# Kernel optimization log

Hardware: AMD Instinct MI355X
Metric: run time of the kernel (lower is better)

## Reference

```python
import jax, jax.numpy as jnp
import numpy as np
import math

D = 2048
NH = 16
HD = D // NH
MULT = 4
EPS = 1e-6


def rmsnorm(x, g):
    norm = jax.lax.rsqrt(jnp.mean(x * x, axis=-1, keepdims=True) + EPS)
    return g * x * norm


def setup_inputs() -> dict:
    key = jax.random.key(0)
    ks = jax.random.split(key, 8)
    s = 0.02  # keep activations in a sane range
    return {
        "x": jax.random.normal(ks[0], (2, 2048, D), dtype=jnp.float32),
        "g1": jnp.ones((D,), dtype=jnp.float32),
        "wq": jax.random.normal(ks[1], (D, D), dtype=jnp.float32) * s,
        "wk": jax.random.normal(ks[2], (D, D), dtype=jnp.float32) * s,
        "wv": jax.random.normal(ks[3], (D, D), dtype=jnp.float32) * s,
        "wo": jax.random.normal(ks[4], (D, D), dtype=jnp.float32) * s,
        "g2": jnp.ones((D,), dtype=jnp.float32),
        "w_up": jax.random.normal(ks[5], (2 * D * MULT, D), dtype=jnp.float32) * s,
        "w_down": jax.random.normal(ks[6], (D, D * MULT), dtype=jnp.float32) * s,
    }


def reference(x, g1, wq, wk, wv, wo, g2, w_up, w_down):
    B, T, _ = x.shape
    # --- causal self-attention with pre-RMSNorm ---
    h = rmsnorm(x, g1)
    q = (h @ wq.T).reshape(B, T, NH, HD).transpose(0, 2, 1, 3)  # [B,H,T,hd]
    k = (h @ wk.T).reshape(B, T, NH, HD).transpose(0, 2, 1, 3)
    v = (h @ wv.T).reshape(B, T, NH, HD).transpose(0, 2, 1, 3)
    att = jnp.einsum("bhtd,bhsd->bhts", q, k) / math.sqrt(HD)  # [B,H,T,T]
    neg = jnp.finfo(att.dtype).min
    causal = jnp.triu(jnp.full((T, T), neg, dtype=att.dtype), k=1)
    att = att + causal
    w = jax.nn.softmax(att, axis=-1)
    z = jnp.einsum("bhts,bhsd->bhtd", w, v)  # [B,H,T,hd]
    z = z.transpose(0, 2, 1, 3).reshape(B, T, D)
    x = x + z @ wo.T
    # --- SwiGLU-style FFN (GELU gate) with pre-RMSNorm ---
    h2 = rmsnorm(x, g2)
    uv = h2 @ w_up.T  # [B,T,2*D*MULT]
    u, vgate = jnp.split(uv, 2, axis=-1)
    ff = (jax.nn.gelu(u, approximate=False) * vgate) @ w_down.T
    return x + ff
```

## Files before the change

### kernel.cpp

```cpp
#include <hip/hip_runtime.h>
#include <math.h>

typedef __bf16 bf16_t;
typedef __bf16 bf16x8 __attribute__((ext_vector_type(8)));
typedef __bf16 bf16x4 __attribute__((ext_vector_type(4)));
typedef float f32x4 __attribute__((ext_vector_type(4)));

#define D_MODEL 2048
#define N_HEADS 16
#define HEAD_D 128
#define SEQ 2048
#define NTOK 4096
#define DFF 8192
#define UPN 16384

#define GLDS16(g, l) __builtin_amdgcn_global_load_lds( \
    (const __attribute__((address_space(1))) void*)(g), \
    (__attribute__((address_space(3))) void*)(l), 16, 0, 0)

#define MFMA16(a, b, c) __builtin_amdgcn_mfma_f32_16x16x32_bf16((a), (b), (c), 0, 0, 0)

__global__ __launch_bounds__(256) void cvt_bf16_kernel(const float* __restrict__ in,
                                                       bf16_t* __restrict__ out, long n4) {
    long i = (long)blockIdx.x * 256 + threadIdx.x;
    long stride = (long)gridDim.x * 256;
    for (; i < n4; i += stride) {
        float4 f = ((const float4*)in)[i];
        bf16x4 v;
        v[0] = (bf16_t)f.x; v[1] = (bf16_t)f.y; v[2] = (bf16_t)f.z; v[3] = (bf16_t)f.w;
        ((bf16x4*)out)[i] = v;
    }
}

__global__ __launch_bounds__(256) void rmsnorm_kernel(const float* __restrict__ x,
                                                      const float* __restrict__ g,
                                                      bf16_t* __restrict__ out) {
    int row = blockIdx.x;
    const float* xr = x + (size_t)row * D_MODEL;
    int c0 = threadIdx.x * 8;
    float4 a = *(const float4*)&xr[c0];
    float4 b = *(const float4*)&xr[c0 + 4];
    float ss = a.x*a.x + a.y*a.y + a.z*a.z + a.w*a.w
             + b.x*b.x + b.y*b.y + b.z*b.z + b.w*b.w;
    #pragma unroll
    for (int off = 1; off < 64; off <<= 1) ss += __shfl_xor(ss, off);
    __shared__ float red[4];
    if ((threadIdx.x & 63) == 0) red[threadIdx.x >> 6] = ss;
    __syncthreads();
    float norm = rsqrtf((red[0] + red[1] + red[2] + red[3]) * (1.f / D_MODEL) + 1e-6f);
    float4 ga = *(const float4*)&g[c0];
    float4 gb = *(const float4*)&g[c0 + 4];
    bf16x8 o;
    o[0] = (bf16_t)(a.x * ga.x * norm); o[1] = (bf16_t)(a.y * ga.y * norm);
    o[2] = (bf16_t)(a.z * ga.z * norm); o[3] = (bf16_t)(a.w * ga.w * norm);
    o[4] = (bf16_t)(b.x * gb.x * norm); o[5] = (bf16_t)(b.y * gb.y * norm);
    o[6] = (bf16_t)(b.z * gb.z * norm); o[7] = (bf16_t)(b.w * gb.w * norm);
    *(bf16x8*)&out[(size_t)row * D_MODEL + c0] = o;
}

__global__ __launch_bounds__(256) void combine3_kernel(const float* __restrict__ r,
        const float* __restrict__ p0, const float* __restrict__ p1,
        float* __restrict__ out, long n4) {
    long i = (long)blockIdx.x * 256 + threadIdx.x;
    long stride = (long)gridDim.x * 256;
    for (; i < n4; i += stride) {
        float4 a = ((const float4*)r)[i];
        float4 b = ((const float4*)p0)[i];
        float4 c = ((const float4*)p1)[i];
        float4 o; o.x = a.x+b.x+c.x; o.y = a.y+b.y+c.y; o.z = a.z+b.z+c.z; o.w = a.w+b.w+c.w;
        ((float4*)out)[i] = o;
    }
}

template<int MODE, int KSPLIT>
__global__ __launch_bounds__(512, 2)
void gemm256(const bf16_t* __restrict__ A, const bf16_t* __restrict__ W,
             void* __restrict__ o0, void* __restrict__ o1, void* __restrict__ o2,
             const float* __restrict__ res, int nbx, int K)
{
    __shared__ __align__(16) bf16_t ldsA[2 * 2 * 8192];
    __shared__ __align__(16) bf16_t ldsB[2 * 2 * 8192];
    const int tid = threadIdx.x;
    const int wave = tid >> 6, lane = tid & 63;
    const int lr = lane & 15, lg = lane >> 4;
    const int wm = wave >> 2, wn = wave & 3;

    const int nwg = gridDim.x, bid = blockIdx.x;
    const int cpx = nwg >> 3;
    const int s = (bid & 7) * cpx + (bid >> 3);
    const int by = s & 15, bx = s >> 4;
    const int bm0 = by * 256;
    const int bn0 = (MODE == 2) ? bx * 128 : bx * 256;
    const int z = (KSPLIT == 2) ? blockIdx.z : 0;
    const int Keff = K / KSPLIT, koff = z * Keff;

    const int rl = wave * 16 + (lane >> 2);
    const int gsw = ((lane & 3) ^ ((rl >> 1) & 3)) * 8;
    const bf16_t* asrc = A + (size_t)(bm0 + rl) * K + koff + gsw;
    const bf16_t* bsrc;
    size_t bstep2;
    if constexpr (MODE == 2) {
        int grp = rl >> 6, wi = rl & 63;
        int brow = (wi < 32) ? (bn0 + grp * 32 + wi) : (DFF + bn0 + grp * 32 + (wi - 32));
        bsrc = W + (size_t)brow * K + koff + gsw;
        bstep2 = (size_t)64 * K;
    } else {
        bsrc = W + (size_t)(bn0 + rl) * K + koff + gsw;
        bstep2 = (size_t)128 * K;
    }

    auto stA = [&](int t, int kh) {
        char* d = (char*)ldsA + (((t & 1) * 2 + kh) * 16384) + wave * 1024 + lane * 16;
        const bf16_t* sp = asrc + (size_t)t * 64 + kh * 32;
        GLDS16(sp, d);
        GLDS16(sp + (size_t)128 * K, d + 8192);
    };
    auto stB = [&](int t, int kh) {
        char* d = (char*)ldsB + (((t & 1) * 2 + kh) * 16384) + wave * 1024 + lane * 16;
        const bf16_t* sp = bsrc + (size_t)t * 64 + kh * 32;
        GLDS16(sp, d);
        GLDS16(sp + bstep2, d + 8192);
    };

    f32x4 acc[8][4] = {};
    const int xg = (lg ^ ((lr >> 1) & 3)) * 8;
    const int NKT = Keff >> 6;

    stA(0, 0); stB(0, 0); stA(0, 1); stB(0, 1); stA(1, 0); stB(1, 0);
    asm volatile("s_waitcnt vmcnt(8)" ::: "memory");
    __builtin_amdgcn_s_barrier();

#define TILE_BODY(T, S1, S2, W1, W2)                                                    \
    {                                                                                   \
        const int t_ = (T);                                                             \
        const bf16_t* Ab = ldsA + ((t_ & 1) * 2) * 8192;                                \
        const bf16_t* Bb = ldsB + ((t_ & 1) * 2) * 8192;                                \
        bf16x8 a0[4], a1[4], b0[4], b1[4];                                              \
                                                                      \
        _Pragma("unroll")                                                               \
        for (int i = 0; i < 4; ++i)                                                     \
            a0[i] = *(const bf16x8*)&Ab[(wm * 128 + i * 16 + lr) * 32 + xg];            \
        _Pragma("unroll")                                                               \
        for (int n = 0; n < 4; ++n)                                                     \
            b0[n] = *(const bf16x8*)&Bb[(wn * 64 + n * 16 + lr) * 32 + xg];             \
        if (S1) stA(t_ + 1, 1);                                                         \
        __builtin_amdgcn_s_setprio(1);                                                  \
        _Pragma("unroll")                                                               \
        for (int i = 0; i < 4; ++i)                                                     \
            _Pragma("unroll")                                                           \
            for (int n = 0; n < 4; ++n)                                                 \
                acc[i][n] = MFMA16(a0[i], b0[n], acc[i][n]);                            \
        __builtin_amdgcn_s_setprio(0);                                                  \
                                                                      \
        _Pragma("unroll")                                                               \
        for (int i = 0; i < 4; ++i)                                                     \
            a1[i] = *(const bf16x8*)&Ab[(wm * 128 + (i + 4) * 16 + lr) * 32 + xg];      \
        if (S1) stB(t_ + 1, 1);                                                         \
        __builtin_amdgcn_s_setprio(1);                                                  \
        _Pragma("unroll")                                                               \
        for (int i = 0; i < 4; ++i)                                                     \
            _Pragma("unroll")                                                           \
            for (int n = 0; n < 4; ++n)                                                 \
                acc[i + 4][n] = MFMA16(a1[i], b0[n], acc[i + 4][n]);                    \
        __builtin_amdgcn_s_setprio(0);                                                  \
        asm volatile("s_waitcnt vmcnt(" W1 ")" ::: "memory");                           \
        __builtin_amdgcn_s_barrier();                                                   \
                                                                      \
        _Pragma("unroll")                                                               \
        for (int i = 0; i < 4; ++i)                                                     \
            a0[i] = *(const bf16x8*)&Ab[8192 + (wm * 128 + i * 16 + lr) * 32 + xg];     \
        _Pragma("unroll")                                                               \
        for (int n = 0; n < 4; ++n)                                                     \
            b1[n] = *(const bf16x8*)&Bb[8192 + (wn * 64 + n * 16 + lr) * 32 + xg];      \
        if (S2) stA(t_ + 2, 0);                                                         \
        __builtin_amdgcn_s_setprio(1);                                                  \
        _Pragma("unroll")                                                               \
        for (int i = 0; i < 4; ++i)                                                     \
            _Pragma("unroll")                                                           \
            for (int n = 0; n < 4; ++n)                                                 \
                acc[i][n] = MFMA16(a0[i], b1[n], acc[i][n]);                            \
        __builtin_amdgcn_s_setprio(0);                                                  \
                                                                      \
        _Pragma("unroll")                                                               \
        for (int i = 0; i < 4; ++i)                                                     \
            a1[i] = *(const bf16x8*)&Ab[8192 + (wm * 128 + (i + 4) * 16 + lr) * 32 + xg]; \
        if (S2) stB(t_ + 2, 0);                                                         \
        __builtin_amdgcn_s_setprio(1);                                                  \
        _Pragma("unroll")                                                               \
        for (int i = 0; i < 4; ++i)                                                     \
            _Pragma("unroll")                                                           \
            for (int n = 0; n < 4; ++n)                                                 \
                acc[i + 4][n] = MFMA16(a1[i], b1[n], acc[i + 4][n]);                    \
        __builtin_amdgcn_s_setprio(0);                                                  \
        asm volatile("s_waitcnt vmcnt(" W2 ")" ::: "memory");                           \
        __builtin_amdgcn_s_barrier();                                                   \
    }

    for (int t = 0; t < NKT - 2; ++t) TILE_BODY(t, true, true, "8", "8");
    TILE_BODY(NKT - 2, true, false, "8", "4");
    TILE_BODY(NKT - 1, false, false, "0", "0");
#undef TILE_BODY

    if constexpr (MODE == 0) {
        const float qs = 0.08838834764831845f;
        const int th = bn0 >> 11;
        #pragma unroll
        for (int m = 0; m < 8; ++m) {
            int grow = bm0 + wm * 128 + m * 16 + lg * 4;
            #pragma unroll
            for (int n = 0; n < 4; ++n) {
                int gcol = bn0 + wn * 64 + n * 16 + lr;
                int c = gcol & 2047;
                if (th == 0) {
                    #pragma unroll
                    for (int r = 0; r < 4; ++r)
                        ((bf16_t*)o0)[(size_t)(grow + r) * D_MODEL + c] = (bf16_t)(acc[m][n][r] * qs);
                } else if (th == 1) {
                    #pragma unroll
                    for (int r = 0; r < 4; ++r)
                        ((bf16_t*)o1)[(size_t)(grow + r) * D_MODEL + c] = (bf16_t)acc[m][n][r];
                } else {
                    int hh = c >> 7, d = c & 127;
                    int bb = grow >> 11, t0 = grow & 2047;
                    bf16x4 st;
                    #pragma unroll
                    for (int r = 0; r < 4; ++r) st[r] = (bf16_t)acc[m][n][r];
                    *(bf16x4*)&((bf16_t*)o2)[((size_t)(bb * N_HEADS + hh) * HEAD_D + d) * SEQ + t0] = st;
                }
            }
        }
    } else if constexpr (MODE == 1) {
        float* po = (KSPLIT == 2) ? ((float*)o0 + (size_t)z * NTOK * D_MODEL) : (float*)o0;
        #pragma unroll
        for (int m = 0; m < 8; ++m) {
            int grow = bm0 + wm * 128 + m * 16 + lg * 4;
            #pragma unroll
            for (int n = 0; n < 4; ++n) {
                int gcol = bn0 + wn * 64 + n * 16 + lr;
                #pragma unroll
                for (int r = 0; r < 4; ++r) {
                    size_t idx = (size_t)(grow + r) * D_MODEL + gcol;
                    if (KSPLIT == 2) po[idx] = acc[m][n][r];
                    else             po[idx] = res[idx] + acc[m][n][r];
                }
            }
        }
    } else {
        #pragma unroll
        for (int m = 0; m < 8; ++m) {
            int grow = bm0 + wm * 128 + m * 16 + lg * 4;
            #pragma unroll
            for (int n = 0; n < 2; ++n) {
                int gcol = bn0 + wn * 32 + n * 16 + lr;
                #pragma unroll
                for (int r = 0; r < 4; ++r) {
                    float u = acc[m][n][r], vg = acc[m][n + 2][r];
                    float ge = 0.5f * u * (1.f + erff(u * 0.70710678118654752f));
                    ((bf16_t*)o0)[(size_t)(grow + r) * DFF + gcol] = (bf16_t)(ge * vg);
                }
            }
        }
    }
}

__global__ __launch_bounds__(256)
void attn_kernel(const bf16_t* __restrict__ Q, const bf16_t* __restrict__ K,
                 const bf16_t* __restrict__ Vt, bf16_t* __restrict__ Z)
{
    const int qt = gridDim.x - 1 - blockIdx.x;
    const int h = blockIdx.y, b = blockIdx.z;
    const int q0 = qt * 64;
    const int tid = threadIdx.x, wave = tid >> 6, lane = tid & 63;
    const int lr = lane & 15, lg = lane >> 4;

    __shared__ __align__(16) bf16_t Qs[64 * 136];
    __shared__ __align__(16) bf16_t Ks[64 * 136];
    __shared__ __align__(16) bf16_t Vts[128 * 72];
    __shared__ __align__(16) bf16_t Ps[4][16 * 72];

    const size_t base = ((size_t)b * SEQ) * D_MODEL + (size_t)h * HEAD_D;
    const size_t vbase = (size_t)(b * N_HEADS + h) * HEAD_D * SEQ;

    const int kr = tid >> 4, kc = (tid & 15) * 8;
    const int vdr = tid >> 3, vc = (tid & 7) * 8;

    #pragma unroll
    for (int i = 0; i < 4; ++i)
        *(uint4*)&Qs[(kr + i * 16) * 136 + kc] =
            *(const uint4*)&Q[base + (size_t)(q0 + kr + i * 16) * D_MODEL + kc];

    uint4 k0g, k1g, k2g, k3g, v0g, v1g, v2g, v3g;
    const bf16_t* Kb = K + base + (size_t)kr * D_MODEL + kc;
    const bf16_t* Vb = Vt + vbase + (size_t)vdr * SEQ + vc;
    auto loadKV = [&](int kt) {
        const bf16_t* kp = Kb + (size_t)kt * 64 * D_MODEL;
        k0g = *(const uint4*)kp;
        k1g = *(const uint4*)(kp + (size_t)16 * D_MODEL);
        k2g = *(const uint4*)(kp + (size_t)32 * D_MODEL);
        k3g = *(const uint4*)(kp + (size_t)48 * D_MODEL);
        const bf16_t* vp = Vb + kt * 64;
        v0g = *(const uint4*)vp;
        v1g = *(const uint4*)(vp + (size_t)32 * SEQ);
        v2g = *(const uint4*)(vp + (size_t)64 * SEQ);
        v3g = *(const uint4*)(vp + (size_t)96 * SEQ);
    };
    loadKV(0);

    f32x4 o[8] = {};
    float mrun[4], lrun[4];
    #pragma unroll
    for (int r = 0; r < 4; ++r) { mrun[r] = -1e30f; lrun[r] = 0.f; }

    for (int kt = 0; kt <= qt; ++kt) {
        __syncthreads();
        *(uint4*)&Ks[kr * 136 + kc] = k0g;
        *(uint4*)&Ks[(kr + 16) * 136 + kc] = k1g;
        *(uint4*)&Ks[(kr + 32) * 136 + kc] = k2g;
        *(uint4*)&Ks[(kr + 48) * 136 + kc] = k3g;
        *(uint4*)&Vts[vdr * 72 + vc] = v0g;
        *(uint4*)&Vts[(vdr + 32) * 72 + vc] = v1g;
        *(uint4*)&Vts[(vdr + 64) * 72 + vc] = v2g;
        *(uint4*)&Vts[(vdr + 96) * 72 + vc] = v3g;
        __syncthreads();
        if (kt < qt) loadKV(kt + 1);

        f32x4 sv[4] = {};
        #pragma unroll
        for (int kk = 0; kk < 4; ++kk) {
            bf16x8 aq = *(const bf16x8*)&Qs[(wave * 16 + lr) * 136 + kk * 32 + lg * 8];
            #pragma unroll
            for (int nb = 0; nb < 4; ++nb) {
                bf16x8 bk = *(const bf16x8*)&Ks[(nb * 16 + lr) * 136 + kk * 32 + lg * 8];
                sv[nb] = MFMA16(aq, bk, sv[nb]);
            }
        }
        if (kt == qt) {
            #pragma unroll
            for (int nb = 0; nb < 4; ++nb)
                #pragma unroll
                for (int r = 0; r < 4; ++r) {
                    int qrel = 16 * wave + lg * 4 + r;
                    int krel = nb * 16 + lr;
                    if (krel > qrel) sv[nb][r] = -1e30f;
                }
        }
        float resc[4];
        bool defer_all = true;
        #pragma unroll
        for (int r = 0; r < 4; ++r) {
            float mx = fmaxf(fmaxf(sv[0][r], sv[1][r]), fmaxf(sv[2][r], sv[3][r]));
            #pragma unroll
            for (int off = 1; off < 16; off <<= 1) mx = fmaxf(mx, __shfl_xor(mx, off));
            bool defer = __all(mx - mrun[r] <= 8.f);
            float mnew = defer ? mrun[r] : fmaxf(mrun[r], mx);
            resc[r] = defer ? 1.f : __expf(mrun[r] - mnew);
            defer_all &= defer;
            float sum = 0.f;
            #pragma unroll
            for (int nb = 0; nb < 4; ++nb) {
                float p = __expf(sv[nb][r] - mnew);
                sv[nb][r] = p;
                sum += p;
            }
            #pragma unroll
            for (int off = 1; off < 16; off <<= 1) sum += __shfl_xor(sum, off);
            lrun[r] = lrun[r] * resc[r] + sum;
            mrun[r] = mnew;
        }
        if (!defer_all) {
            #pragma unroll
            for (int ob = 0; ob < 8; ++ob)
                #pragma unroll
                for (int r = 0; r < 4; ++r) o[ob][r] *= resc[r];
        }
        #pragma unroll
        for (int nb = 0; nb < 4; ++nb)
            #pragma unroll
            for (int r = 0; r < 4; ++r)
                Ps[wave][(lg * 4 + r) * 72 + nb * 16 + lr] = (bf16_t)sv[nb][r];
        #pragma unroll
        for (int kk = 0; kk < 2; ++kk) {
            bf16x8 ap = *(const bf16x8*)&Ps[wave][lr * 72 + kk * 32 + lg * 8];
            #pragma unroll
            for (int ob = 0; ob < 8; ++ob) {
                bf16x8 bv = *(const bf16x8*)&Vts[(ob * 16 + lr) * 72 + kk * 32 + lg * 8];
                o[ob] = MFMA16(ap, bv, o[ob]);
            }
        }
    }
    #pragma unroll
    for (int r = 0; r < 4; ++r) lrun[r] = 1.f / lrun[r];
    #pragma unroll
    for (int ob = 0; ob < 8; ++ob)
        #pragma unroll
        for (int r = 0; r < 4; ++r) {
            int t = q0 + 16 * wave + lg * 4 + r;
            Z[base + (size_t)t * D_MODEL + ob * 16 + lr] = (bf16_t)(o[ob][r] * lrun[r]);
        }
}

extern "C" void kernel_launch(void* const* d_in, const int* in_sizes, int n_in,
                              void* d_out, int out_size, void* d_ws, size_t ws_size,
                              hipStream_t stream)
{
    const float* x   = (const float*)d_in[0];
    const float* g1  = (const float*)d_in[1];
    const float* wq  = (const float*)d_in[2];
    const float* wk  = (const float*)d_in[3];
    const float* wv  = (const float*)d_in[4];
    const float* wo  = (const float*)d_in[5];
    const float* g2  = (const float*)d_in[6];
    const float* wup = (const float*)d_in[7];
    const float* wdn = (const float*)d_in[8];
    float* out = (float*)d_out;

    char* wsp = (char*)d_ws;
    size_t off = 0;
    auto alloc = [&](size_t bytes) { void* p = wsp + off; off += (bytes + 255) & ~255ull; return p; };
    bf16_t* wq_b  = (bf16_t*)alloc((size_t)D_MODEL * D_MODEL * 2);
    bf16_t* wk_b  = (bf16_t*)alloc((size_t)D_MODEL * D_MODEL * 2);
    bf16_t* wv_b  = (bf16_t*)alloc((size_t)D_MODEL * D_MODEL * 2);
    bf16_t* wo_b  = (bf16_t*)alloc((size_t)D_MODEL * D_MODEL * 2);
    bf16_t* wup_b = (bf16_t*)alloc((size_t)UPN * D_MODEL * 2);
    bf16_t* wdn_b = (bf16_t*)alloc((size_t)D_MODEL * DFF * 2);
    bf16_t* h_b   = (bf16_t*)alloc((size_t)NTOK * D_MODEL * 2);
    bf16_t* q_b   = (bf16_t*)alloc((size_t)NTOK * D_MODEL * 2);
    bf16_t* k_b   = (bf16_t*)alloc((size_t)NTOK * D_MODEL * 2);
    bf16_t* vt_b  = (bf16_t*)alloc((size_t)NTOK * D_MODEL * 2);
    bf16_t* z_b   = (bf16_t*)alloc((size_t)NTOK * D_MODEL * 2);
    float*  x1    = (float*) alloc((size_t)NTOK * D_MODEL * 4);
    bf16_t* h2_b  = (bf16_t*)alloc((size_t)NTOK * D_MODEL * 2);
    bf16_t* act_b = (bf16_t*)alloc((size_t)NTOK * DFF * 2);
    float* pbuf = (float*)h_b;

    auto cvt = [&](const float* in, bf16_t* outb, long n) {
        long n4 = n / 4;
        long nb = (n4 + 255) / 256;
        int blocks = nb > 2048 ? 2048 : (int)nb;
        cvt_bf16_kernel<<<blocks, 256, 0, stream>>>(in, outb, n4);
    };
    cvt(wq,  wq_b,  (long)D_MODEL * D_MODEL);
    cvt(wk,  wk_b,  (long)D_MODEL * D_MODEL);
    cvt(wv,  wv_b,  (long)D_MODEL * D_MODEL);
    cvt(wo,  wo_b,  (long)D_MODEL * D_MODEL);
    cvt(wup, wup_b, (long)UPN * D_MODEL);
    cvt(wdn, wdn_b, (long)D_MODEL * DFF);

    rmsnorm_kernel<<<NTOK, 256, 0, stream>>>(x, g1, h_b);

    gemm256<0, 1><<<24 * 16, 512, 0, stream>>>(h_b, wq_b, q_b, k_b, vt_b, nullptr, 24, D_MODEL);

    attn_kernel<<<dim3(SEQ / 64, N_HEADS, 2), 256, 0, stream>>>(q_b, k_b, vt_b, z_b);

    gemm256<1, 2><<<dim3(8 * 16, 1, 2), 512, 0, stream>>>(z_b, wo_b, pbuf, nullptr, nullptr, nullptr, 8, D_MODEL);
    combine3_kernel<<<2048, 256, 0, stream>>>(x, pbuf, pbuf + (size_t)NTOK * D_MODEL, x1,
                                              (long)NTOK * D_MODEL / 4);

    rmsnorm_kernel<<<NTOK, 256, 0, stream>>>(x1, g2, h2_b);

    gemm256<2, 1><<<64 * 16, 512, 0, stream>>>(h2_b, wup_b, act_b, nullptr, nullptr, nullptr, 64, D_MODEL);

    gemm256<1, 2><<<dim3(8 * 16, 1, 2), 512, 0, stream>>>(act_b, wdn_b, pbuf, nullptr, nullptr, nullptr, 8, DFF);
    combine3_kernel<<<2048, 256, 0, stream>>>(x1, pbuf, pbuf + (size_t)NTOK * D_MODEL, out,
                                              (long)NTOK * D_MODEL / 4);
}
```

Measured before the change: 963.4 us.

## Store split-K partials in bf16, fuse residual add with RMSNorm, widen attention query tile

Split-K GEMM partial outputs are now written as bf16 rather than fp32, which halves the traffic for the partial buffers and their readback in the combine kernels. The first residual combine is fused with the second RMSNorm into one row kernel, removing one launch and one full pass over x1. The attention kernel now handles 128 query rows per block as two 64-row halves that share each K/V tile load, and the V tile's LDS row pitch changes from 72 to 68. Rounding the partials to bf16 before summing costs accuracy in the residual stream, and the larger attention tile raises register and LDS use.

```diff
diff --git a/kernel.cpp b/kernel.cpp
--- a/kernel.cpp
+++ b/kernel.cpp
@@ -59,17 +59,67 @@
 }
 
 __global__ __launch_bounds__(256) void combine3_kernel(const float* __restrict__ r,
-        const float* __restrict__ p0, const float* __restrict__ p1,
-        float* __restrict__ out, long n4) {
+        const bf16_t* __restrict__ p0, const bf16_t* __restrict__ p1,
+        float* __restrict__ out, long n8) {
     long i = (long)blockIdx.x * 256 + threadIdx.x;
     long stride = (long)gridDim.x * 256;
-    for (; i < n4; i += stride) {
-        float4 a = ((const float4*)r)[i];
-        float4 b = ((const float4*)p0)[i];
-        float4 c = ((const float4*)p1)[i];
-        float4 o; o.x = a.x+b.x+c.x; o.y = a.y+b.y+c.y; o.z = a.z+b.z+c.z; o.w = a.w+b.w+c.w;
-        ((float4*)out)[i] = o;
-    }
+    for (; i < n8; i += stride) {
+        size_t e = (size_t)i * 8;
+        float4 a0 = *(const float4*)&r[e];
+        float4 a1 = *(const float4*)&r[e + 4];
+        bf16x8 b0 = *(const bf16x8*)&p0[e];
+        bf16x8 b1 = *(const bf16x8*)&p1[e];
+        float4 o0, o1;
+        o0.x = a0.x + (float)b0[0] + (float)b1[0];
+        o0.y = a0.y + (float)b0[1] + (float)b1[1];
+        o0.z = a0.z + (float)b0[2] + (float)b1[2];
+        o0.w = a0.w + (float)b0[3] + (float)b1[3];
+        o1.x = a1.x + (float)b0[4] + (float)b1[4];
+        o1.y = a1.y + (float)b0[5] + (float)b1[5];
+        o1.z = a1.z + (float)b0[6] + (float)b1[6];
+        o1.w = a1.w + (float)b0[7] + (float)b1[7];
+        *(float4*)&out[e] = o0;
+        *(float4*)&out[e + 4] = o1;
+    }
+}
+
+__global__ __launch_bounds__(256) void combine_rms_kernel(const float* __restrict__ r,
+        const bf16_t* __restrict__ p0, const bf16_t* __restrict__ p1,
+        const float* __restrict__ g, float* __restrict__ x1, bf16_t* __restrict__ h2) {
+    int row = blockIdx.x;
+    size_t rb = (size_t)row * D_MODEL;
+    int c0 = threadIdx.x * 8;
+    float4 a0 = *(const float4*)&r[rb + c0];
+    float4 a1 = *(const float4*)&r[rb + c0 + 4];
+    bf16x8 b0 = *(const bf16x8*)&p0[rb + c0];
+    bf16x8 b1 = *(const bf16x8*)&p1[rb + c0];
+    float v0 = a0.x + (float)b0[0] + (float)b1[0];
+    float v1 = a0.y + (float)b0[1] + (float)b1[1];
+    float v2 = a0.z + (float)b0[2] + (float)b1[2];
+    float v3 = a0.w + (float)b0[3] + (float)b1[3];
+    float v4 = a1.x + (float)b0[4] + (float)b1[4];
+    float v5 = a1.y + (float)b0[5] + (float)b1[5];
+    float v6 = a1.z + (float)b0[6] + (float)b1[6];
+    float v7 = a1.w + (float)b0[7] + (float)b1[7];
+    float4 w0; w0.x = v0; w0.y = v1; w0.z = v2; w0.w = v3;
+    float4 w1; w1.x = v4; w1.y = v5; w1.z = v6; w1.w = v7;
+    *(float4*)&x1[rb + c0] = w0;
+    *(float4*)&x1[rb + c0 + 4] = w1;
+    float ss = v0*v0 + v1*v1 + v2*v2 + v3*v3 + v4*v4 + v5*v5 + v6*v6 + v7*v7;
+    #pragma unroll
+    for (int off = 1; off < 64; off <<= 1) ss += __shfl_xor(ss, off);
+    __shared__ float red[4];
+    if ((threadIdx.x & 63) == 0) red[threadIdx.x >> 6] = ss;
+    __syncthreads();
+    float norm = rsqrtf((red[0] + red[1] + red[2] + red[3]) * (1.f / D_MODEL) + 1e-6f);
+    float4 ga = *(const float4*)&g[c0];
+    float4 gb = *(const float4*)&g[c0 + 4];
+    bf16x8 o;
+    o[0] = (bf16_t)(v0 * ga.x * norm); o[1] = (bf16_t)(v1 * ga.y * norm);
+    o[2] = (bf16_t)(v2 * ga.z * norm); o[3] = (bf16_t)(v3 * ga.w * norm);
+    o[4] = (bf16_t)(v4 * gb.x * norm); o[5] = (bf16_t)(v5 * gb.y * norm);
+    o[6] = (bf16_t)(v6 * gb.z * norm); o[7] = (bf16_t)(v7 * gb.w * norm);
+    *(bf16x8*)&h2[rb + c0] = o;
 }
 
 template<int MODE, int KSPLIT>
@@ -230,7 +280,7 @@
             }
         }
     } else if constexpr (MODE == 1) {
-        float* po = (KSPLIT == 2) ? ((float*)o0 + (size_t)z * NTOK * D_MODEL) : (float*)o0;
+        bf16_t* po = (bf16_t*)o0 + (size_t)z * NTOK * D_MODEL;
         #pragma unroll
         for (int m = 0; m < 8; ++m) {
             int grow = bm0 + wm * 128 + m * 16 + lg * 4;
@@ -240,8 +290,7 @@
                 #pragma unroll
                 for (int r = 0; r < 4; ++r) {
                     size_t idx = (size_t)(grow + r) * D_MODEL + gcol;
-                    if (KSPLIT == 2) po[idx] = acc[m][n][r];
-                    else             po[idx] = res[idx] + acc[m][n][r];
+                    po[idx] = (bf16_t)acc[m][n][r];
                 }
             }
         }
@@ -263,19 +312,64 @@
     }
 }
 
+#define SM_PV(svv, mr, lrr, oo)                                                         \
+    {                                                                                   \
+        float resc_[4]; bool dall_ = true;                                              \
+        _Pragma("unroll")                                                               \
+        for (int r = 0; r < 4; ++r) {                                                   \
+            float mx = fmaxf(fmaxf(svv[0][r], svv[1][r]), fmaxf(svv[2][r], svv[3][r]));  \
+            _Pragma("unroll")                                                           \
+            for (int off = 1; off < 16; off <<= 1) mx = fmaxf(mx, __shfl_xor(mx, off)); \
+            bool defer = __all(mx - mr[r] <= 8.f);                                      \
+            float mnew = defer ? mr[r] : fmaxf(mr[r], mx);                              \
+            resc_[r] = defer ? 1.f : __expf(mr[r] - mnew);                              \
+            dall_ &= defer;                                                             \
+            float sum = 0.f;                                                            \
+            _Pragma("unroll")                                                           \
+            for (int nb = 0; nb < 4; ++nb) {                                            \
+                float p = __expf(svv[nb][r] - mnew);                                    \
+                svv[nb][r] = p; sum += p;                                               \
+            }                                                                           \
+            _Pragma("unroll")                                                           \
+            for (int off = 1; off < 16; off <<= 1) sum += __shfl_xor(sum, off);         \
+            lrr[r] = lrr[r] * resc_[r] + sum; mr[r] = mnew;                             \
+        }                                                                               \
+        if (!dall_) {                                                                   \
+            _Pragma("unroll")                                                           \
+            for (int ob = 0; ob < 8; ++ob)                                              \
+                _Pragma("unroll")                                                       \
+                for (int r = 0; r < 4; ++r) oo[ob][r] *= resc_[r];                      \
+        }                                                                               \
+        _Pragma("unroll")                                                               \
+        for (int nb = 0; nb < 4; ++nb)                                                  \
+            _Pragma("unroll")                                                           \
+            for (int r = 0; r < 4; ++r)                                                 \
+                Ps[wave][(lg * 4 + r) * 72 + nb * 16 + lr] = (bf16_t)svv[nb][r];        \
+        _Pragma("unroll")                                                               \
+        for (int kk = 0; kk < 2; ++kk) {                                                \
+            bf16x8 ap = *(const bf16x8*)&Ps[wave][lr * 72 + kk * 32 + lg * 8];          \
+            _Pragma("unroll")                                                           \
+            for (int ob = 0; ob < 8; ++ob) {                                            \
+                bf16x8 bv = *(const bf16x8*)&Vts[(ob * 16 + lr) * 68 + kk * 32 + lg * 8]; \
+                oo[ob] = MFMA16(ap, bv, oo[ob]);                                        \
+            }                                                                           \
+        }                                                                               \
+    }
+
 __global__ __launch_bounds__(256)
 void attn_kernel(const bf16_t* __restrict__ Q, const bf16_t* __restrict__ K,
                  const bf16_t* __restrict__ Vt, bf16_t* __restrict__ Z)
 {
-    const int qt = gridDim.x - 1 - blockIdx.x;
+    const int qb = gridDim.x - 1 - blockIdx.x;
     const int h = blockIdx.y, b = blockIdx.z;
-    const int q0 = qt * 64;
+    const int q0 = qb * 128;
+    const int ktmax = 2 * qb + 1;
     const int tid = threadIdx.x, wave = tid >> 6, lane = tid & 63;
     const int lr = lane & 15, lg = lane >> 4;
 
-    __shared__ __align__(16) bf16_t Qs[64 * 136];
+    __shared__ __align__(16) bf16_t Qs[128 * 136];
     __shared__ __align__(16) bf16_t Ks[64 * 136];
-    __shared__ __align__(16) bf16_t Vts[128 * 72];
+    __shared__ __align__(16) bf16_t Vts[128 * 68];
     __shared__ __align__(16) bf16_t Ps[4][16 * 72];
 
     const size_t base = ((size_t)b * SEQ) * D_MODEL + (size_t)h * HEAD_D;
@@ -285,7 +379,7 @@
     const int vdr = tid >> 3, vc = (tid & 7) * 8;
 
     #pragma unroll
-    for (int i = 0; i < 4; ++i)
+    for (int i = 0; i < 8; ++i)
         *(uint4*)&Qs[(kr + i * 16) * 136 + kc] =
             *(const uint4*)&Q[base + (size_t)(q0 + kr + i * 16) * D_MODEL + kc];
 
@@ -306,98 +400,83 @@
     };
     loadKV(0);
 
-    f32x4 o[8] = {};
-    float mrun[4], lrun[4];
+    f32x4 oL[8] = {}, oH[8] = {};
+    float mL[4], lL[4], mH[4], lH[4];
     #pragma unroll
-    for (int r = 0; r < 4; ++r) { mrun[r] = -1e30f; lrun[r] = 0.f; }
-
-    for (int kt = 0; kt <= qt; ++kt) {
+    for (int r = 0; r < 4; ++r) { mL[r] = -1e30f; lL[r] = 0.f; mH[r] = -1e30f; lH[r] = 0.f; }
+
+    for (int kt = 0; kt <= ktmax; ++kt) {
         __syncthreads();
         *(uint4*)&Ks[kr * 136 + kc] = k0g;
         *(uint4*)&Ks[(kr + 16) * 136 + kc] = k1g;
         *(uint4*)&Ks[(kr + 32) * 136 + kc] = k2g;
         *(uint4*)&Ks[(kr + 48) * 136 + kc] = k3g;
-        *(uint4*)&Vts[vdr * 72 + vc] = v0g;
-        *(uint4*)&Vts[(vdr + 32) * 72 + vc] = v1g;
-        *(uint4*)&Vts[(vdr + 64) * 72 + vc] = v2g;
-        *(uint4*)&Vts[(vdr + 96) * 72 + vc] = v3g;
+        *(uint4*)&Vts[vdr * 68 + vc] = v0g;
+        *(uint4*)&Vts[(vdr + 32) * 68 + vc] = v1g;
+        *(uint4*)&Vts[(vdr + 64) * 68 + vc] = v2g;
+        *(uint4*)&Vts[(vdr + 96) * 68 + vc] = v3g;
         __syncthreads();
-        if (kt < qt) loadKV(kt + 1);
-
-        f32x4 sv[4] = {};
-        #pragma unroll
-        for (int kk = 0; kk < 4; ++kk) {
-            bf16x8 aq = *(const bf16x8*)&Qs[(wave * 16 + lr) * 136 + kk * 32 + lg * 8];
+        if (kt < ktmax) loadKV(kt + 1);
+
+        if (kt < ktmax) {
+            f32x4 sv[4] = {};
             #pragma unroll
-            for (int nb = 0; nb < 4; ++nb) {
-                bf16x8 bk = *(const bf16x8*)&Ks[(nb * 16 + lr) * 136 + kk * 32 + lg * 8];
-                sv[nb] = MFMA16(aq, bk, sv[nb]);
-            }
+            for (int kk = 0; kk < 4; ++kk) {
+                bf16x8 aq = *(const bf16x8*)&Qs[(wave * 16 + lr) * 136 + kk * 32 + lg * 8];
+                #pragma unroll
+                for (int nb = 0; nb < 4; ++nb) {
+                    bf16x8 bk = *(const bf16x8*)&Ks[(nb * 16 + lr) * 136 + kk * 32 + lg * 8];
+                    sv[nb] = MFMA16(aq, bk, sv[nb]);
+                }
+            }
+            if (kt == ktmax - 1) {
+                #pragma unroll
+                for (int nb = 0; nb < 4; ++nb)
+                    #pragma unroll
+                    for (int r = 0; r < 4; ++r) {
+                        int qrel = 16 * wave + lg * 4 + r;
+                        int krel = nb * 16 + lr;
+                        if (krel > qrel) sv[nb][r] = -1e30f;
+                    }
+            }
+            SM_PV(sv, mL, lL, oL)
         }
-        if (kt == qt) {
+        {
+            f32x4 sv[4] = {};
             #pragma unroll
-            for (int nb = 0; nb < 4; ++nb)
+            for (int kk = 0; kk < 4; ++kk) {
+                bf16x8 aq = *(const bf16x8*)&Qs[(64 + wave * 16 + lr) * 136 + kk * 32 + lg * 8];
                 #pragma unroll
-                for (int r = 0; r < 4; ++r) {
-                    int qrel = 16 * wave + lg * 4 + r;
-                    int krel = nb * 16 + lr;
-                    if (krel > qrel) sv[nb][r] = -1e30f;
+                for (int nb = 0; nb < 4; ++nb) {
+                    bf16x8 bk = *(const bf16x8*)&Ks[(nb * 16 + lr) * 136 + kk * 32 + lg * 8];
+                    sv[nb] = MFMA16(aq, bk, sv[nb]);
                 }
+            }
+            if (kt == ktmax) {
+                #pragma unroll
+                for (int nb = 0; nb < 4; ++nb)
+                    #pragma unroll
+                    for (int r = 0; r < 4; ++r) {
+                        int qrel = 16 * wave + lg * 4 + r;
+                        int krel = nb * 16 + lr;
+                        if (krel > qrel) sv[nb][r] = -1e30f;
+                    }
+            }
+            SM_PV(sv, mH, lH, oH)
         }
-        float resc[4];
-        bool defer_all = true;
-        #pragma unroll
-        for (int r = 0; r < 4; ++r) {
-            float mx = fmaxf(fmaxf(sv[0][r], sv[1][r]), fmaxf(sv[2][r], sv[3][r]));
-            #pragma unroll
-            for (int off = 1; off < 16; off <<= 1) mx = fmaxf(mx, __shfl_xor(mx, off));
-            bool defer = __all(mx - mrun[r] <= 8.f);
-            float mnew = defer ? mrun[r] : fmaxf(mrun[r], mx);
-            resc[r] = defer ? 1.f : __expf(mrun[r] - mnew);
-            defer_all &= defer;
-            float sum = 0.f;
-            #pragma unroll
-            for (int nb = 0; nb < 4; ++nb) {
-                float p = __expf(sv[nb][r] - mnew);
-                sv[nb][r] = p;
-                sum += p;
-            }
-            #pragma unroll
-            for (int off = 1; off < 16; off <<= 1) sum += __shfl_xor(sum, off);
-            lrun[r] = lrun[r] * resc[r] + sum;
-            mrun[r] = mnew;
-        }
-        if (!defer_all) {
-            #pragma unroll
-            for (int ob = 0; ob < 8; ++ob)
-                #pragma unroll
-                for (int r = 0; r < 4; ++r) o[ob][r] *= resc[r];
-        }
-        #pragma unroll
-        for (int nb = 0; nb < 4; ++nb)
-            #pragma unroll
-            for (int r = 0; r < 4; ++r)
-                Ps[wave][(lg * 4 + r) * 72 + nb * 16 + lr] = (bf16_t)sv[nb][r];
-        #pragma unroll
-        for (int kk = 0; kk < 2; ++kk) {
-            bf16x8 ap = *(const bf16x8*)&Ps[wave][lr * 72 + kk * 32 + lg * 8];
-            #pragma unroll
-            for (int ob = 0; ob < 8; ++ob) {
-                bf16x8 bv = *(const bf16x8*)&Vts[(ob * 16 + lr) * 72 + kk * 32 + lg * 8];
-                o[ob] = MFMA16(ap, bv, o[ob]);
-            }
-        }
     }
     #pragma unroll
-    for (int r = 0; r < 4; ++r) lrun[r] = 1.f / lrun[r];
+    for (int r = 0; r < 4; ++r) { lL[r] = 1.f / lL[r]; lH[r] = 1.f / lH[r]; }
     #pragma unroll
     for (int ob = 0; ob < 8; ++ob)
         #pragma unroll
         for (int r = 0; r < 4; ++r) {
             int t = q0 + 16 * wave + lg * 4 + r;
-            Z[base + (size_t)t * D_MODEL + ob * 16 + lr] = (bf16_t)(o[ob][r] * lrun[r]);
+            Z[base + (size_t)t * D_MODEL + ob * 16 + lr] = (bf16_t)(oL[ob][r] * lL[r]);
+            Z[base + (size_t)(t + 64) * D_MODEL + ob * 16 + lr] = (bf16_t)(oH[ob][r] * lH[r]);
         }
 }
+#undef SM_PV
 
 extern "C" void kernel_launch(void* const* d_in, const int* in_sizes, int n_in,
                               void* d_out, int out_size, void* d_ws, size_t ws_size,
@@ -431,7 +510,7 @@
     float*  x1    = (float*) alloc((size_t)NTOK * D_MODEL * 4);
     bf16_t* h2_b  = (bf16_t*)alloc((size_t)NTOK * D_MODEL * 2);
     bf16_t* act_b = (bf16_t*)alloc((size_t)NTOK * DFF * 2);
-    float* pbuf = (float*)h_b;
+    bf16_t* pbuf = h_b;
 
     auto cvt = [&](const float* in, bf16_t* outb, long n) {
         long n4 = n / 4;
@@ -450,17 +529,14 @@
 
     gemm256<0, 1><<<24 * 16, 512, 0, stream>>>(h_b, wq_b, q_b, k_b, vt_b, nullptr, 24, D_MODEL);
 
-    attn_kernel<<<dim3(SEQ / 64, N_HEADS, 2), 256, 0, stream>>>(q_b, k_b, vt_b, z_b);
+    attn_kernel<<<dim3(SEQ / 128, N_HEADS, 2), 256, 0, stream>>>(q_b, k_b, vt_b, z_b);
 
     gemm256<1, 2><<<dim3(8 * 16, 1, 2), 512, 0, stream>>>(z_b, wo_b, pbuf, nullptr, nullptr, nullptr, 8, D_MODEL);
-    combine3_kernel<<<2048, 256, 0, stream>>>(x, pbuf, pbuf + (size_t)NTOK * D_MODEL, x1,
-                                              (long)NTOK * D_MODEL / 4);
-
-    rmsnorm_kernel<<<NTOK, 256, 0, stream>>>(x1, g2, h2_b);
+    combine_rms_kernel<<<NTOK, 256, 0, stream>>>(x, pbuf, pbuf + (size_t)NTOK * D_MODEL, g2, x1, h2_b);
 
     gemm256<2, 1><<<64 * 16, 512, 0, stream>>>(h2_b, wup_b, act_b, nullptr, nullptr, nullptr, 64, D_MODEL);
 
     gemm256<1, 2><<<dim3(8 * 16, 1, 2), 512, 0, stream>>>(act_b, wdn_b, pbuf, nullptr, nullptr, nullptr, 8, DFF);
     combine3_kernel<<<2048, 256, 0, stream>>>(x1, pbuf, pbuf + (size_t)NTOK * D_MODEL, out,
-                                              (long)NTOK * D_MODEL / 4);
-}
+                                              (long)NTOK * D_MODEL / 8);
+}
```

Result: faster. 930.1 us (-3.5%).
